# Kernel optimization log

Hardware: AMD Instinct MI355X
Metric: run time of the kernel (lower is better)

## Reference

```python
import jax, jax.numpy as jnp
import numpy as np

NUM_ATTRS = 8    # A: number of attribute names in attr_map
NUM_VALS = 16    # V: number of distinct values per attribute


def setup_inputs() -> dict:
    key = jax.random.key(0)
    k1, k2 = jax.random.split(key)
    B, D = 2_000_000, 8
    predictions = jax.random.normal(k1, (B, D), dtype=jnp.float32)
    attr_vals = jax.random.randint(k2, (B, NUM_ATTRS), 0, NUM_VALS, dtype=jnp.int32)
    return {"predictions": predictions, "attr_vals": attr_vals}


def reference(predictions, attr_vals):
    B, A = attr_vals.shape
    V = NUM_VALS
    # per-node mean of sigmoid probs; stacking rows then .mean() == mean of per-node means
    per_node = jnp.mean(jax.nn.sigmoid(predictions), axis=1)  # [B]
    # flatten (attr, value) groups into A*V segments
    seg_ids = (attr_vals + jnp.arange(A, dtype=attr_vals.dtype)[None, :] * V).reshape(-1)  # [B*A]
    vals = jnp.broadcast_to(per_node[:, None], (B, A)).reshape(-1)  # [B*A]
    sums = jax.ops.segment_sum(vals, seg_ids, num_segments=A * V)
    counts = jax.ops.segment_sum(jnp.ones_like(vals), seg_ids, num_segments=A * V)
    means = (sums / jnp.maximum(counts, 1.0)).reshape(A, V)      # [A, V]
    present = (counts > 0).reshape(A, V)                          # [A, V]
    # pairwise squared diffs of group means within each attribute (i < j)
    diff = means[:, :, None] - means[:, None, :]                  # [A, V, V]
    triu = jnp.triu(jnp.ones((V, V), dtype=bool), k=1)
    pair_mask = present[:, :, None] & present[:, None, :] & triu[None, :, :]
    total_loss = jnp.sum(jnp.where(pair_mask, diff * diff, 0.0))
    num_comparisons = jnp.sum(pair_mask)
    return jnp.where(num_comparisons > 0, total_loss / num_comparisons, 0.0)
```

## Files before the change

kernel.cpp:

```cpp
#include <hip/hip_runtime.h>

#define NA 8
#define NV 16
#define NS (NA * NV)
#define FIX_SHIFT 43
#define FIX_MASK ((1ULL << FIX_SHIFT) - 1)
#define FIX_SCALE 2147483648.0f

__global__ __launch_bounds__(256) void k1_accum(
    const float* __restrict__ preds,
    const int*   __restrict__ attrs,
    unsigned long long* __restrict__ partials,
    int B, int nb)
{
    __shared__ unsigned long long h[NS];
    for (int i = threadIdx.x; i < NS; i += 256) h[i] = 0ULL;
    __syncthreads();

    const int stride = nb * 256;
    for (int r = blockIdx.x * 256 + threadIdx.x; r < B; r += stride) {
        const float4* p4 = (const float4*)(preds + (size_t)r * NA);
        float4 p0 = p4[0];
        float4 p1 = p4[1];

        float s = __builtin_amdgcn_rcpf(1.0f + __expf(-p0.x))
                + __builtin_amdgcn_rcpf(1.0f + __expf(-p0.y))
                + __builtin_amdgcn_rcpf(1.0f + __expf(-p0.z))
                + __builtin_amdgcn_rcpf(1.0f + __expf(-p0.w))
                + __builtin_amdgcn_rcpf(1.0f + __expf(-p1.x))
                + __builtin_amdgcn_rcpf(1.0f + __expf(-p1.y))
                + __builtin_amdgcn_rcpf(1.0f + __expf(-p1.z))
                + __builtin_amdgcn_rcpf(1.0f + __expf(-p1.w));
        float per_node = s * 0.125f;
        unsigned int fixed = (unsigned int)(per_node * FIX_SCALE);
        unsigned long long add = (1ULL << FIX_SHIFT) | (unsigned long long)fixed;

        const int4* a4 = (const int4*)(attrs + (size_t)r * NA);
        int4 a0 = a4[0];
        int4 a1 = a4[1];

        atomicAdd(&h[0 * NV + a0.x], add);
        atomicAdd(&h[1 * NV + a0.y], add);
        atomicAdd(&h[2 * NV + a0.z], add);
        atomicAdd(&h[3 * NV + a0.w], add);
        atomicAdd(&h[4 * NV + a1.x], add);
        atomicAdd(&h[5 * NV + a1.y], add);
        atomicAdd(&h[6 * NV + a1.z], add);
        atomicAdd(&h[7 * NV + a1.w], add);
    }
    __syncthreads();

    if (threadIdx.x < NS) {
        partials[(size_t)threadIdx.x * nb + blockIdx.x] = h[threadIdx.x];
    }
}

__global__ __launch_bounds__(256) void k2_reduce(
    const unsigned long long* __restrict__ partials,
    double* __restrict__ means,
    int*    __restrict__ pres,
    int nb)
{
    const int s = blockIdx.x;
    unsigned long long sum = 0ULL;
    unsigned int cnt = 0u;
    for (int b = threadIdx.x; b < nb; b += 256) {
        unsigned long long p = partials[(size_t)s * nb + b];
        cnt += (unsigned int)(p >> FIX_SHIFT);
        sum += (p & FIX_MASK);
    }
    for (int off = 32; off > 0; off >>= 1) {
        sum += __shfl_down(sum, off, 64);
        cnt += __shfl_down(cnt, off, 64);
    }
    __shared__ unsigned long long ws_[4];
    __shared__ unsigned int wc_[4];
    const int wave = threadIdx.x >> 6;
    if ((threadIdx.x & 63) == 0) { ws_[wave] = sum; wc_[wave] = cnt; }
    __syncthreads();
    if (threadIdx.x == 0) {
        unsigned long long S = ws_[0] + ws_[1] + ws_[2] + ws_[3];
        unsigned int C = wc_[0] + wc_[1] + wc_[2] + wc_[3];
        means[s] = C ? ((double)S * (1.0 / (double)FIX_SCALE)) / (double)C : 0.0;
        pres[s]  = C ? 1 : 0;
    }
}

__global__ __launch_bounds__(128) void k3_finalize(
    const double* __restrict__ means,
    const int*    __restrict__ pres,
    float* __restrict__ out)
{
    __shared__ double s_mean[NS];
    __shared__ int    s_pres[NS];
    const int t = threadIdx.x;
    s_mean[t] = means[t];
    s_pres[t] = pres[t];
    __syncthreads();

    const int a = t >> 4;
    const int i = t & (NV - 1);
    double loss = 0.0;
    int    ncmp = 0;
    if (s_pres[t]) {
        const double mi = s_mean[t];
        for (int j = i + 1; j < NV; ++j) {
            const int sj = a * NV + j;
            if (s_pres[sj]) {
                const double d = mi - s_mean[sj];
                loss += d * d;
                ncmp += 1;
            }
        }
    }
    for (int off = 32; off > 0; off >>= 1) {
        loss += __shfl_down(loss, off, 64);
        ncmp += __shfl_down(ncmp, off, 64);
    }
    __shared__ double w_loss[2];
    __shared__ int    w_ncmp[2];
    const int wave = t >> 6;
    if ((t & 63) == 0) { w_loss[wave] = loss; w_ncmp[wave] = ncmp; }
    __syncthreads();
    if (t == 0) {
        const double total = w_loss[0] + w_loss[1];
        const int    n     = w_ncmp[0] + w_ncmp[1];
        out[0] = (n > 0) ? (float)(total / (double)n) : 0.0f;
    }
}

extern "C" void kernel_launch(void* const* d_in, const int* in_sizes, int n_in,
                              void* d_out, int out_size, void* d_ws, size_t ws_size,
                              hipStream_t stream) {
    const float* preds = (const float*)d_in[0];
    const int*   attrs = (const int*)d_in[1];
    float*       out   = (float*)d_out;

    const int B = in_sizes[1] / NA;

    const size_t tail = NS * sizeof(double) + NS * sizeof(int);
    int nb = 1024;
    if (ws_size < (size_t)NS * 1024 * sizeof(unsigned long long) + tail) nb = 512;

    unsigned long long* partials = (unsigned long long*)d_ws;
    double* means = (double*)((char*)d_ws + (size_t)NS * nb * sizeof(unsigned long long));
    int*    pres  = (int*)(means + NS);

    k1_accum<<<nb, 256, 0, stream>>>(preds, attrs, partials, B, nb);
    k2_reduce<<<NS, 256, 0, stream>>>(partials, means, pres, nb);
    k3_finalize<<<1, 128, 0, stream>>>(means, pres, out);
}
```

Before: 146.4 us.

## Privatize LDS histogram per wave, process two rows per thread, raise block count

Each wave gets its own copy of the shared-memory histogram, which cuts contention on LDS atomics between the waves of a block; the copies are summed at the end. Each thread now handles two consecutive rows per iteration with wider vector loads, giving more memory-level parallelism, and the grid can grow to 2048 blocks when the workspace is large enough. The costs are four times the LDS, more partials for the second kernel to reduce, and higher register use per thread.

Measured after the change: 149.0 us. Within noise of the previous version (+1.8%).

```diff
diff --git a/kernel.cpp b/kernel.cpp
--- a/kernel.cpp
+++ b/kernel.cpp
@@ -3,9 +3,23 @@
 #define NA 8
 #define NV 16
 #define NS (NA * NV)
+#define NW 4
 #define FIX_SHIFT 43
 #define FIX_MASK ((1ULL << FIX_SHIFT) - 1)
 #define FIX_SCALE 2147483648.0f
+
+
+__device__ __forceinline__ float sigmoid8_mean(float4 p0, float4 p1) {
+    float s = __builtin_amdgcn_rcpf(1.0f + __expf(-p0.x))
+            + __builtin_amdgcn_rcpf(1.0f + __expf(-p0.y))
+            + __builtin_amdgcn_rcpf(1.0f + __expf(-p0.z))
+            + __builtin_amdgcn_rcpf(1.0f + __expf(-p0.w))
+            + __builtin_amdgcn_rcpf(1.0f + __expf(-p1.x))
+            + __builtin_amdgcn_rcpf(1.0f + __expf(-p1.y))
+            + __builtin_amdgcn_rcpf(1.0f + __expf(-p1.z))
+            + __builtin_amdgcn_rcpf(1.0f + __expf(-p1.w));
+    return s * 0.125f;
+}
 
 __global__ __launch_bounds__(256) void k1_accum(
     const float* __restrict__ preds,
@@ -13,45 +27,84 @@
     unsigned long long* __restrict__ partials,
     int B, int nb)
 {
-    __shared__ unsigned long long h[NS];
-    for (int i = threadIdx.x; i < NS; i += 256) h[i] = 0ULL;
-    __syncthreads();
-
-    const int stride = nb * 256;
-    for (int r = blockIdx.x * 256 + threadIdx.x; r < B; r += stride) {
+    __shared__ unsigned long long h[NW][NS];
+    for (int i = threadIdx.x; i < NW * NS; i += 256)
+        ((unsigned long long*)h)[i] = 0ULL;
+    __syncthreads();
+
+    const int wave = threadIdx.x >> 6;
+    unsigned long long* __restrict__ hw = h[wave];
+
+    const int stride  = nb * 256;
+    const int npairs  = B >> 1;
+
+    for (int rp = blockIdx.x * 256 + threadIdx.x; rp < npairs; rp += stride) {
+        const int r0 = rp * 2;
+        const float4* p4 = (const float4*)(preds + (size_t)r0 * NA);
+        float4 p0 = p4[0];
+        float4 p1 = p4[1];
+        float4 p2 = p4[2];
+        float4 p3 = p4[3];
+        const int4* a4 = (const int4*)(attrs + (size_t)r0 * NA);
+        int4 a0 = a4[0];
+        int4 a1 = a4[1];
+        int4 a2 = a4[2];
+        int4 a3 = a4[3];
+
+        {
+            float per_node = sigmoid8_mean(p0, p1);
+            unsigned int fixed = (unsigned int)(per_node * FIX_SCALE);
+            unsigned long long add = (1ULL << FIX_SHIFT) | (unsigned long long)fixed;
+            atomicAdd(&hw[0 * NV + a0.x], add);
+            atomicAdd(&hw[1 * NV + a0.y], add);
+            atomicAdd(&hw[2 * NV + a0.z], add);
+            atomicAdd(&hw[3 * NV + a0.w], add);
+            atomicAdd(&hw[4 * NV + a1.x], add);
+            atomicAdd(&hw[5 * NV + a1.y], add);
+            atomicAdd(&hw[6 * NV + a1.z], add);
+            atomicAdd(&hw[7 * NV + a1.w], add);
+        }
+        {
+            float per_node = sigmoid8_mean(p2, p3);
+            unsigned int fixed = (unsigned int)(per_node * FIX_SCALE);
+            unsigned long long add = (1ULL << FIX_SHIFT) | (unsigned long long)fixed;
+            atomicAdd(&hw[0 * NV + a2.x], add);
+            atomicAdd(&hw[1 * NV + a2.y], add);
+            atomicAdd(&hw[2 * NV + a2.z], add);
+            atomicAdd(&hw[3 * NV + a2.w], add);
+            atomicAdd(&hw[4 * NV + a3.x], add);
+            atomicAdd(&hw[5 * NV + a3.y], add);
+            atomicAdd(&hw[6 * NV + a3.z], add);
+            atomicAdd(&hw[7 * NV + a3.w], add);
+        }
+    }
+
+    if ((B & 1) && blockIdx.x == 0 && threadIdx.x == 0) {
+        const int r = B - 1;
         const float4* p4 = (const float4*)(preds + (size_t)r * NA);
         float4 p0 = p4[0];
         float4 p1 = p4[1];
-
-        float s = __builtin_amdgcn_rcpf(1.0f + __expf(-p0.x))
-                + __builtin_amdgcn_rcpf(1.0f + __expf(-p0.y))
-                + __builtin_amdgcn_rcpf(1.0f + __expf(-p0.z))
-                + __builtin_amdgcn_rcpf(1.0f + __expf(-p0.w))
-                + __builtin_amdgcn_rcpf(1.0f + __expf(-p1.x))
-                + __builtin_amdgcn_rcpf(1.0f + __expf(-p1.y))
-                + __builtin_amdgcn_rcpf(1.0f + __expf(-p1.z))
-                + __builtin_amdgcn_rcpf(1.0f + __expf(-p1.w));
-        float per_node = s * 0.125f;
+        float per_node = sigmoid8_mean(p0, p1);
         unsigned int fixed = (unsigned int)(per_node * FIX_SCALE);
         unsigned long long add = (1ULL << FIX_SHIFT) | (unsigned long long)fixed;
-
         const int4* a4 = (const int4*)(attrs + (size_t)r * NA);
         int4 a0 = a4[0];
         int4 a1 = a4[1];
-
-        atomicAdd(&h[0 * NV + a0.x], add);
-        atomicAdd(&h[1 * NV + a0.y], add);
-        atomicAdd(&h[2 * NV + a0.z], add);
-        atomicAdd(&h[3 * NV + a0.w], add);
-        atomicAdd(&h[4 * NV + a1.x], add);
-        atomicAdd(&h[5 * NV + a1.y], add);
-        atomicAdd(&h[6 * NV + a1.z], add);
-        atomicAdd(&h[7 * NV + a1.w], add);
+        atomicAdd(&hw[0 * NV + a0.x], add);
+        atomicAdd(&hw[1 * NV + a0.y], add);
+        atomicAdd(&hw[2 * NV + a0.z], add);
+        atomicAdd(&hw[3 * NV + a0.w], add);
+        atomicAdd(&hw[4 * NV + a1.x], add);
+        atomicAdd(&hw[5 * NV + a1.y], add);
+        atomicAdd(&hw[6 * NV + a1.z], add);
+        atomicAdd(&hw[7 * NV + a1.w], add);
     }
     __syncthreads();
 
     if (threadIdx.x < NS) {
-        partials[(size_t)threadIdx.x * nb + blockIdx.x] = h[threadIdx.x];
+        unsigned long long m = h[0][threadIdx.x] + h[1][threadIdx.x]
+                             + h[2][threadIdx.x] + h[3][threadIdx.x];
+        partials[(size_t)threadIdx.x * nb + blockIdx.x] = m;
     }
 }
 
@@ -139,8 +192,11 @@
     const int B = in_sizes[1] / NA;
 
     const size_t tail = NS * sizeof(double) + NS * sizeof(int);
-    int nb = 1024;
-    if (ws_size < (size_t)NS * 1024 * sizeof(unsigned long long) + tail) nb = 512;
+    int nb = 2048;
+    while (nb > 512 &&
+           ws_size < (size_t)NS * nb * sizeof(unsigned long long) + tail) {
+        nb >>= 1;
+    }
 
     unsigned long long* partials = (unsigned long long*)d_ws;
     double* means = (double*)((char*)d_ws + (size_t)NS * nb * sizeof(unsigned long long));
```

## Split rows across lane pairs for coalesced loads, per-wave histograms, prefetch

Applied to the files above, without the earlier changes.

Each row is now handled by two adjacent lanes. Each lane loads one float4 of predictions and one int4 of attributes, so a wave reads contiguous 1 KB chunks, and the two half-sums are combined with a lane shuffle. Shared-memory histograms are replicated per wave to cut atomic contention, a software prefetch of the next chunk overlaps loads with the atomics, and the grid grows to up to 2048 blocks. The costs are more shared memory, a shuffle per row, a larger partials array for the reduce kernel, and special handling for tail rows when B is not a multiple of 32.

After: 153.9 us. 5.1% more time.

```diff
diff --git a/kernel.cpp b/kernel.cpp
--- a/kernel.cpp
+++ b/kernel.cpp
@@ -3,9 +3,30 @@
 #define NA 8
 #define NV 16
 #define NS (NA * NV)
+#define NW 4
 #define FIX_SHIFT 43
 #define FIX_MASK ((1ULL << FIX_SHIFT) - 1)
 #define FIX_SCALE 2147483648.0f
+
+
+__device__ __forceinline__ float sig(float x) {
+    return __builtin_amdgcn_rcpf(1.0f + __expf(-x));
+}
+
+__device__ __forceinline__ void process_chunk(
+    float4 p, int4 a, int lane, unsigned long long* __restrict__ hw)
+{
+    float hs = sig(p.x) + sig(p.y) + sig(p.z) + sig(p.w);
+    float s  = hs + __shfl_xor(hs, 1, 64);
+    float per_node = s * 0.125f;
+    unsigned int fixed = (unsigned int)(per_node * FIX_SCALE);
+    unsigned long long add = (1ULL << FIX_SHIFT) | (unsigned long long)fixed;
+    const int abase = (lane & 1) << 2;
+    atomicAdd(&hw[((abase + 0) << 4) + a.x], add);
+    atomicAdd(&hw[((abase + 1) << 4) + a.y], add);
+    atomicAdd(&hw[((abase + 2) << 4) + a.z], add);
+    atomicAdd(&hw[((abase + 3) << 4) + a.w], add);
+}
 
 __global__ __launch_bounds__(256) void k1_accum(
     const float* __restrict__ preds,
@@ -13,45 +34,53 @@
     unsigned long long* __restrict__ partials,
     int B, int nb)
 {
-    __shared__ unsigned long long h[NS];
-    for (int i = threadIdx.x; i < NS; i += 256) h[i] = 0ULL;
+    __shared__ unsigned long long h[NW][NS];
+    for (int i = threadIdx.x; i < NW * NS; i += 256)
+        ((unsigned long long*)h)[i] = 0ULL;
     __syncthreads();
 
-    const int stride = nb * 256;
-    for (int r = blockIdx.x * 256 + threadIdx.x; r < B; r += stride) {
-        const float4* p4 = (const float4*)(preds + (size_t)r * NA);
-        float4 p0 = p4[0];
-        float4 p1 = p4[1];
+    const int lane = threadIdx.x & 63;
+    const int wave = threadIdx.x >> 6;
+    unsigned long long* __restrict__ hw = h[wave];
 
-        float s = __builtin_amdgcn_rcpf(1.0f + __expf(-p0.x))
-                + __builtin_amdgcn_rcpf(1.0f + __expf(-p0.y))
-                + __builtin_amdgcn_rcpf(1.0f + __expf(-p0.z))
-                + __builtin_amdgcn_rcpf(1.0f + __expf(-p0.w))
-                + __builtin_amdgcn_rcpf(1.0f + __expf(-p1.x))
-                + __builtin_amdgcn_rcpf(1.0f + __expf(-p1.y))
-                + __builtin_amdgcn_rcpf(1.0f + __expf(-p1.z))
-                + __builtin_amdgcn_rcpf(1.0f + __expf(-p1.w));
-        float per_node = s * 0.125f;
-        unsigned int fixed = (unsigned int)(per_node * FIX_SCALE);
-        unsigned long long add = (1ULL << FIX_SHIFT) | (unsigned long long)fixed;
+    const float4* __restrict__ p4 = (const float4*)preds;
+    const int4*   __restrict__ a4 = (const int4*)attrs;
 
-        const int4* a4 = (const int4*)(attrs + (size_t)r * NA);
-        int4 a0 = a4[0];
-        int4 a1 = a4[1];
+    const int gw      = blockIdx.x * NW + wave;
+    const int nwv     = nb * NW;
+    const int nchunks = B >> 5;
 
-        atomicAdd(&h[0 * NV + a0.x], add);
-        atomicAdd(&h[1 * NV + a0.y], add);
-        atomicAdd(&h[2 * NV + a0.z], add);
-        atomicAdd(&h[3 * NV + a0.w], add);
-        atomicAdd(&h[4 * NV + a1.x], add);
-        atomicAdd(&h[5 * NV + a1.y], add);
-        atomicAdd(&h[6 * NV + a1.z], add);
-        atomicAdd(&h[7 * NV + a1.w], add);
+    int c = gw;
+    if (c < nchunks) {
+        float4 p = p4[(size_t)c * 64 + lane];
+        int4   a = a4[(size_t)c * 64 + lane];
+        for (;;) {
+            const int  cn   = c + nwv;
+            const bool more = (cn < nchunks);
+            float4 pn; int4 an;
+            if (more) {
+                pn = p4[(size_t)cn * 64 + lane];
+                an = a4[(size_t)cn * 64 + lane];
+            }
+            process_chunk(p, a, lane, hw);
+            if (!more) break;
+            p = pn; a = an; c = cn;
+        }
+    }
+
+    const int rem = B & 31;
+    if (rem && blockIdx.x == 0 && wave == 0 && lane < rem * 2) {
+        const size_t base = (size_t)(B >> 5) * 64;
+        float4 p = p4[base + lane];
+        int4   a = a4[base + lane];
+        process_chunk(p, a, lane, hw);
     }
     __syncthreads();
 
     if (threadIdx.x < NS) {
-        partials[(size_t)threadIdx.x * nb + blockIdx.x] = h[threadIdx.x];
+        unsigned long long m = h[0][threadIdx.x] + h[1][threadIdx.x]
+                             + h[2][threadIdx.x] + h[3][threadIdx.x];
+        partials[(size_t)threadIdx.x * nb + blockIdx.x] = m;
     }
 }
 
@@ -139,8 +168,11 @@
     const int B = in_sizes[1] / NA;
 
     const size_t tail = NS * sizeof(double) + NS * sizeof(int);
-    int nb = 1024;
-    if (ws_size < (size_t)NS * 1024 * sizeof(unsigned long long) + tail) nb = 512;
+    int nb = 2048;
+    while (nb > 512 &&
+           ws_size < (size_t)NS * nb * sizeof(unsigned long long) + tail) {
+        nb >>= 1;
+    }
 
     unsigned long long* partials = (unsigned long long*)d_ws;
     double* means = (double*)((char*)d_ws + (size_t)NS * nb * sizeof(unsigned long long));
```
